# Optimization experiments

Hardware: AMD Instinct MI355X
Metric: run time of the kernel (lower is better)

Reference implementation:

```python
import jax, jax.numpy as jnp
import numpy as np

D_MODEL = 1024
N_HEADS = 16
HEAD_DIM = D_MODEL // N_HEADS


def setup_inputs() -> dict:
    key = jax.random.key(0)
    k_x, k_wqkv, k_bqkv, k_wout, k_bout = jax.random.split(key, 5)
    s = 1.0 / np.sqrt(D_MODEL)
    return {
        "x": jax.random.normal(k_x, (4, 2048, D_MODEL), dtype=jnp.float32),
        "W_qkv": jax.random.normal(k_wqkv, (D_MODEL, 3 * D_MODEL), dtype=jnp.float32) * s,
        "b_qkv": jax.random.normal(k_bqkv, (3 * D_MODEL,), dtype=jnp.float32) * 0.01,
        "W_out": jax.random.normal(k_wout, (D_MODEL, D_MODEL), dtype=jnp.float32) * s,
        "b_out": jax.random.normal(k_bout, (D_MODEL,), dtype=jnp.float32) * 0.01,
    }


def reference(x, W_qkv, b_qkv, W_out, b_out):
    B, T, D = x.shape
    H, Hd = N_HEADS, HEAD_DIM
    qkv = x @ W_qkv + b_qkv                          # [B,T,3D]
    qkv = qkv.reshape(B, T, 3, H, Hd)
    q, k, v = (qkv[:, :, i].transpose(0, 2, 1, 3) for i in range(3))  # [B,H,T,Hd]
    scale = 1.0 / np.sqrt(Hd)
    attn = jnp.einsum("bhqd,bhkd->bhqk", q, k) * scale  # [B,H,T,T]
    causal = jnp.tril(jnp.ones((T, T), dtype=bool))
    attn = jnp.where(causal, attn, -jnp.inf)
    attn = jax.nn.softmax(attn, axis=-1)
    out = jnp.einsum("bhqk,bhkd->bhqd", attn, v)     # [B,H,T,Hd]
    out = out.transpose(0, 2, 1, 3).reshape(B, T, D)
    return out @ W_out + b_out
```

## Files before the change

kernel.cpp:

```cpp
#include <hip/hip_runtime.h>
#include <hip/hip_bf16.h>
#include <string.h>


typedef unsigned short u16;
typedef unsigned int u32;
typedef __bf16 bf16x8 __attribute__((ext_vector_type(8)));
typedef float f32x4 __attribute__((ext_vector_type(4)));

#define MFMA16(a, b, c) __builtin_amdgcn_mfma_f32_16x16x32_bf16((a), (b), (c), 0, 0, 0)

__device__ __forceinline__ u16 f2bf(float f) {
  unsigned u = __float_as_uint(f);
  u += 0x7fffu + ((u >> 16) & 1u);
  return (u16)(u >> 16);
}

__device__ __forceinline__ u32 pk2bf(float a, float b) {
  __hip_bfloat162 h = __float22bfloat162_rn(make_float2(a, b));
  u32 r;
  memcpy(&r, &h, 4);
  return r;
}

__device__ __forceinline__ void gload_lds16(const void* g, void* l) {
  __builtin_amdgcn_global_load_lds((const __attribute__((address_space(1))) void*)g,
                                   (__attribute__((address_space(3))) void*)l, 16, 0, 0);
}

__global__ __launch_bounds__(256) void cast_x_kernel(const float* __restrict__ x,
                                                     u16* __restrict__ xb) {
  int i = blockIdx.x * 256 + threadIdx.x;
  float4 v = ((const float4*)x)[i];
  ushort4 o;
  o.x = f2bf(v.x); o.y = f2bf(v.y); o.z = f2bf(v.z); o.w = f2bf(v.w);
  ((ushort4*)xb)[i] = o;
}

__global__ __launch_bounds__(256) void tcast_kernel(const float* __restrict__ W,
                                                    u16* __restrict__ Wt, int K, int N) {
  __shared__ float tile[32][33];
  int n0 = blockIdx.x * 32, k0 = blockIdx.y * 32;
  int tx = threadIdx.x & 31, ty = threadIdx.x >> 5;
#pragma unroll
  for (int i = 0; i < 4; i++) {
    int k = ty + i * 8;
    tile[k][tx] = W[(size_t)(k0 + k) * N + n0 + tx];
  }
  __syncthreads();
#pragma unroll
  for (int i = 0; i < 4; i++) {
    int n = ty + i * 8;
    Wt[(size_t)(n0 + n) * K + k0 + tx] = f2bf(tile[tx][n]);
  }
}

__global__ __launch_bounds__(512, 2) void gemm_qkv_kernel(const u16* __restrict__ A,
                                                          const u16* __restrict__ Bt,
                                                          const float* __restrict__ bias,
                                                          u16* __restrict__ QKV) {
  __shared__ u16 As[2][256 * 64];
  __shared__ u16 Bs[2][256 * 64];
  const int tid = threadIdx.x, w = tid >> 6, lane = tid & 63;
  const int g = lane >> 4, c = lane & 15;
  const int wr = w >> 2, wc = w & 3;
  const int m0 = blockIdx.y * 256, n0 = blockIdx.x * 256;
  const int srow = lane >> 3;
  const int sch = (lane & 7) ^ srow;
  const int cx = c & 15 & 7;
  const int wrow = w * 8;

  const u16* gA = A + (size_t)(m0 + wrow + srow) * 1024 + sch * 8;
  const u16* gB = Bt + (size_t)(n0 + wrow + srow) * 1024 + sch * 8;

  auto stageA = [&](int buf, int half, int t) {
#pragma unroll
    for (int i = 0; i < 2; i++)
      gload_lds16(gA + (size_t)(half * 128 + i * 64) * 1024 + t * 64,
                  (char*)(As[buf]) + (half * 128 + i * 64 + wrow) * 128);
  };
  auto stageB = [&](int buf, int half, int t) {
#pragma unroll
    for (int i = 0; i < 2; i++)
      gload_lds16(gB + (size_t)(half * 128 + i * 64) * 1024 + t * 64,
                  (char*)(Bs[buf]) + (half * 128 + i * 64 + wrow) * 128);
  };

  f32x4 acc[8][4];
#pragma unroll
  for (int i = 0; i < 8; i++)
#pragma unroll
    for (int j = 0; j < 4; j++) acc[i][j] = (f32x4){0.f, 0.f, 0.f, 0.f};

  stageB(0, 0, 0);
  stageB(0, 1, 0);
  stageA(0, 0, 0);
  stageA(0, 1, 0);
  stageB(1, 0, 1);
  asm volatile("s_waitcnt vmcnt(2)" ::: "memory");
  __builtin_amdgcn_s_barrier();
  __builtin_amdgcn_sched_barrier(0);

  for (int t = 0; t < 16; t++) {
    const int cur = t & 1;
    const u16* Ab = As[cur];
    const u16* Bb = Bs[cur];
    bf16x8 bf[4][2];
#pragma unroll
    for (int q = 0; q < 4; q++) {
      if (q == 0) {
#pragma unroll
        for (int nt = 0; nt < 4; nt++)
#pragma unroll
          for (int kk = 0; kk < 2; kk++)
            bf[nt][kk] = *(const bf16x8*)(Bb + (wc * 64 + nt * 16 + c) * 64 +
                                          ((kk * 4 + g) ^ cx) * 8);
      }
      bf16x8 af[2][2];
#pragma unroll
      for (int mt = 0; mt < 2; mt++)
#pragma unroll
        for (int kk = 0; kk < 2; kk++)
          af[mt][kk] = *(const bf16x8*)(Ab + (wr * 128 + q * 32 + mt * 16 + c) * 64 +
                                        ((kk * 4 + g) ^ cx) * 8);

      if (q == 0) {
        if (t + 1 < 16) stageB((t + 1) & 1, 1, t + 1);
      } else if (q == 1) {
        if (t + 1 < 16) stageA((t + 1) & 1, 0, t + 1);
      } else if (q == 2) {
        if (t + 1 < 16) stageA((t + 1) & 1, 1, t + 1);
      } else {
        if (t + 2 < 16) stageB(t & 1, 0, t + 2);
      }

      __builtin_amdgcn_sched_barrier(0);
      __builtin_amdgcn_s_barrier();
      asm volatile("s_waitcnt lgkmcnt(0)" ::: "memory");
      __builtin_amdgcn_sched_barrier(0);

      __builtin_amdgcn_s_setprio(1);
#pragma unroll
      for (int mt = 0; mt < 2; mt++)
#pragma unroll
        for (int nt = 0; nt < 4; nt++)
#pragma unroll
          for (int kk = 0; kk < 2; kk++)
            acc[q * 2 + mt][nt] = MFMA16(af[mt][kk], bf[nt][kk], acc[q * 2 + mt][nt]);
      __builtin_amdgcn_s_setprio(0);

      if (q == 3) {
        if (t + 2 < 16) {
          asm volatile("s_waitcnt vmcnt(2)" ::: "memory");
        } else if (t + 1 < 16) {
          asm volatile("s_waitcnt vmcnt(0)" ::: "memory");
        }
      }
      __builtin_amdgcn_sched_barrier(0);
      __builtin_amdgcn_s_barrier();
      __builtin_amdgcn_sched_barrier(0);
    }
  }

  const float qscale = (n0 < 1024) ? 0.18033688011112042f : 1.0f;
  float bn[4];
#pragma unroll
  for (int nt = 0; nt < 4; nt++) bn[nt] = bias[n0 + wc * 64 + nt * 16 + c];
#pragma unroll
  for (int mtg = 0; mtg < 8; mtg++) {
#pragma unroll
    for (int r = 0; r < 4; r++) {
      int m = m0 + wr * 128 + mtg * 16 + g * 4 + r;
      int bb = m >> 11, tk = m & 2047;
#pragma unroll
      for (int nt = 0; nt < 4; nt++) {
        int n = n0 + wc * 64 + nt * 16 + c;
        int which = n >> 10, rem = n & 1023, h = rem >> 6, d = rem & 63;
        float v = (acc[mtg][nt][r] + bn[nt]) * qscale;
        QKV[(size_t)which * 8388608 + (((size_t)(bb * 16 + h) * 2048 + tk) * 64 + d)] = f2bf(v);
      }
    }
  }
}

__global__ __launch_bounds__(256) void vtrans_kernel(const u16* __restrict__ V,
                                                     u16* __restrict__ Vt) {
  __shared__ u16 tile[64][65];
  int bh = blockIdx.y;
  int kt = blockIdx.x;
  int t0 = kt * 64;
  int tx = threadIdx.x & 63, ty = threadIdx.x >> 6;
  const u16* src = V + ((size_t)bh * 2048 + t0) * 64;
#pragma unroll
  for (int i = 0; i < 16; i++) {
    int tr = i * 4 + ty;
    tile[tr][tx] = src[tr * 64 + tx];
  }
  __syncthreads();
  u16* dst = Vt + ((size_t)(bh * 32 + kt)) * 4096;
#pragma unroll
  for (int i = 0; i < 16; i++) {
    int d = i * 4 + ty;
    dst[d * 64 + tx] = tile[tx][d];
  }
}

__global__ __launch_bounds__(512, 4) void attn_kernel(const u16* __restrict__ Q,
                                                      const u16* __restrict__ K,
                                                      const u16* __restrict__ Vt,
                                                      u16* __restrict__ ctx) {
  const int pr = blockIdx.x;
  const int qtA = pr, qtB = 15 - pr;
  const int h = blockIdx.y, b = blockIdx.z;
  const int bh = b * 16 + h;
  const int tid = threadIdx.x, w = tid >> 6, lane = tid & 63;
  const int g = lane >> 4, c = lane & 15;

  const u16* Kg = K + (size_t)bh * 2048 * 64;
  const u16* Vg = Vt + (size_t)bh * 32 * 4096;

  __shared__ u16 Ks[2][64 * 64];
  __shared__ u16 Vs[2][64 * 64];
  __shared__ u32 Pw[8][16 * 32];
  u32* pw = Pw[w];

  const int srow = lane >> 3;
  const int schunk = (lane & 7) ^ (srow & 7);
  const int cx = c & 7;
  const int off0 = ((g ^ cx) * 8);
  const int off1 = (((g ^ cx) ^ 4) * 8);
  const int sw = cx << 2;

  bf16x8 onesf;
#pragma unroll
  for (int i = 0; i < 8; i++) onesf[i] = (__bf16)1.0f;

  const u16* QgA = Q + ((size_t)bh * 2048 + qtA * 128) * 64;
  bf16x8 aq0 = *(const bf16x8*)(QgA + (w * 16 + c) * 64 + g * 8);
  bf16x8 aq1 = *(const bf16x8*)(QgA + (w * 16 + c) * 64 + 32 + g * 8);

  {
    int rbase = w * 8;
    gload_lds16(Kg + (size_t)(rbase + srow) * 64 + schunk * 8, (char*)(Ks[0]) + rbase * 128);
    gload_lds16(Vg + (size_t)(rbase + srow) * 64 + schunk * 8, (char*)(Vs[0]) + rbase * 128);
  }
  __syncthreads();

  f32x4 o[4], la;
#pragma unroll
  for (int nt = 0; nt < 4; nt++) o[nt] = (f32x4){0.f, 0.f, 0.f, 0.f};
  la = (f32x4){0.f, 0.f, 0.f, 0.f};

  const int nA = 2 * qtA + 2;

  auto store_tile = [&](int qbase) {
    float inv = 1.f / la[0];
    int q = qbase + w * 16 + c;
    size_t base = ((size_t)(b * 2048 + q)) * 1024 + h * 64;
#pragma unroll
    for (int nt = 0; nt < 4; nt++) {
      u32 lo = pk2bf(o[nt][0] * inv, o[nt][1] * inv);
      u32 hi = pk2bf(o[nt][2] * inv, o[nt][3] * inv);
      *(uint2*)(ctx + base + nt * 16 + g * 4) = make_uint2(lo, hi);
    }
  };

  for (int r = 0; r < 34; r++) {
    if (r) __syncthreads();

    if (r < 33) {
      const int ktn = (r + 1 < nA) ? (r + 1) : (r + 1 - nA);
      const int nb = (r + 1) & 1;
      int rbase = w * 8;
      gload_lds16(Kg + (size_t)ktn * 4096 + (size_t)(rbase + srow) * 64 + schunk * 8,
                  (char*)(Ks[nb]) + rbase * 128);
      gload_lds16(Vg + (size_t)ktn * 4096 + (size_t)(rbase + srow) * 64 + schunk * 8,
                  (char*)(Vs[nb]) + rbase * 128);
    }

    const bool inA = (r < nA);
    const int kt = inA ? r : (r - nA);
    const int qbase = inA ? qtA * 128 : qtB * 128;
    const int sb0 = qbase + w * 16;
    const int kb = kt * 64;

    if (kb <= sb0 + 15) {
      const u16* Kb = Ks[r & 1];
      const u16* Vb = Vs[r & 1];

      f32x4 sa[4];
#pragma unroll
      for (int nt = 0; nt < 4; nt++) {
        bf16x8 k0 = *(const bf16x8*)(Kb + (nt * 16 + c) * 64 + off0);
        bf16x8 k1 = *(const bf16x8*)(Kb + (nt * 16 + c) * 64 + off1);
        f32x4 z = (f32x4){0.f, 0.f, 0.f, 0.f};
        z = MFMA16(k0, aq0, z);
        z = MFMA16(k1, aq1, z);
        sa[nt] = z;
      }

      const bool domask = (kb + 63 > sb0);
      float pe[4][4];
#pragma unroll
      for (int nt = 0; nt < 4; nt++)
#pragma unroll
        for (int rr = 0; rr < 4; rr++) {
          float t = sa[nt][rr];
          if (domask && (kb + nt * 16 + g * 4 + rr) > (sb0 + c)) t = -1e30f;
          pe[nt][rr] = __builtin_amdgcn_exp2f(t);
        }
#pragma unroll
      for (int nt = 0; nt < 4; nt++) {
        u32 lo = pk2bf(pe[nt][0], pe[nt][1]);
        u32 hi = pk2bf(pe[nt][2], pe[nt][3]);
        *(uint2*)(pw + c * 32 + ((nt * 8 + g * 2) ^ sw)) = make_uint2(lo, hi);
      }
      bf16x8 pB0 = *(const bf16x8*)(pw + c * 32 + ((g * 4) ^ sw));
      bf16x8 pB1 = *(const bf16x8*)(pw + c * 32 + ((16 + g * 4) ^ sw));

      la = MFMA16(onesf, pB0, la);
      la = MFMA16(onesf, pB1, la);

#pragma unroll
      for (int nt = 0; nt < 4; nt++) {
        bf16x8 v0 = *(const bf16x8*)(Vb + (nt * 16 + c) * 64 + off0);
        bf16x8 v1 = *(const bf16x8*)(Vb + (nt * 16 + c) * 64 + off1);
        o[nt] = MFMA16(v0, pB0, o[nt]);
        o[nt] = MFMA16(v1, pB1, o[nt]);
      }
    }

    if (r == nA - 1) {
      store_tile(qtA * 128);
#pragma unroll
      for (int nt = 0; nt < 4; nt++) o[nt] = (f32x4){0.f, 0.f, 0.f, 0.f};
      la = (f32x4){0.f, 0.f, 0.f, 0.f};
      const u16* QgB = Q + ((size_t)bh * 2048 + qtB * 128) * 64;
      aq0 = *(const bf16x8*)(QgB + (w * 16 + c) * 64 + g * 8);
      aq1 = *(const bf16x8*)(QgB + (w * 16 + c) * 64 + 32 + g * 8);
    }
  }

  store_tile(qtB * 128);
}

__global__ __launch_bounds__(256) void gemm_proj_kernel(const u16* __restrict__ A,
                                                        const u16* __restrict__ Bt,
                                                        const float* __restrict__ bias,
                                                        float* __restrict__ out) {
  __shared__ u16 As[128 * 64];
  __shared__ u16 Bs[128 * 64];
  const int tid = threadIdx.x, w = tid >> 6, lane = tid & 63;
  const int g = lane >> 4, c = lane & 15;
  const int wr = w >> 1, wc = w & 1;
  const int m0 = blockIdx.y * 128, n0 = blockIdx.x * 128;
  const int srow = lane >> 3;
  const int sch = (lane & 7) ^ srow;
  const int cx = c & 7;

  f32x4 acc[4][4];
#pragma unroll
  for (int i = 0; i < 4; i++)
#pragma unroll
    for (int j = 0; j < 4; j++) acc[i][j] = (f32x4){0.f, 0.f, 0.f, 0.f};

  for (int k0 = 0; k0 < 1024; k0 += 64) {
    __syncthreads();
#pragma unroll
    for (int i = 0; i < 4; i++) {
      int row = w * 32 + i * 8;
      gload_lds16(A + (size_t)(m0 + row + srow) * 1024 + k0 + sch * 8,
                  (char*)As + row * 128);
      gload_lds16(Bt + (size_t)(n0 + row + srow) * 1024 + k0 + sch * 8,
                  (char*)Bs + row * 128);
    }
    __syncthreads();

#pragma unroll
    for (int kk = 0; kk < 2; kk++) {
      bf16x8 af[4], bf[4];
#pragma unroll
      for (int mt = 0; mt < 4; mt++)
        af[mt] = *(const bf16x8*)(As + (wr * 64 + mt * 16 + c) * 64 + ((kk * 4 + g) ^ cx) * 8);
#pragma unroll
      for (int nt = 0; nt < 4; nt++)
        bf[nt] = *(const bf16x8*)(Bs + (wc * 64 + nt * 16 + c) * 64 + ((kk * 4 + g) ^ cx) * 8);
#pragma unroll
      for (int mt = 0; mt < 4; mt++)
#pragma unroll
        for (int nt = 0; nt < 4; nt++) acc[mt][nt] = MFMA16(af[mt], bf[nt], acc[mt][nt]);
    }
  }

  float bn[4];
#pragma unroll
  for (int nt = 0; nt < 4; nt++) bn[nt] = bias[n0 + wc * 64 + nt * 16 + c];
#pragma unroll
  for (int mt = 0; mt < 4; mt++)
#pragma unroll
    for (int r = 0; r < 4; r++) {
      int m = m0 + wr * 64 + mt * 16 + g * 4 + r;
#pragma unroll
      for (int nt = 0; nt < 4; nt++) {
        int n = n0 + wc * 64 + nt * 16 + c;
        out[(size_t)m * 1024 + n] = acc[mt][nt][r] + bn[nt];
      }
    }
}

extern "C" void kernel_launch(void* const* d_in, const int* in_sizes, int n_in,
                              void* d_out, int out_size, void* d_ws, size_t ws_size,
                              hipStream_t stream) {
  const float* x = (const float*)d_in[0];
  const float* Wqkv = (const float*)d_in[1];
  const float* bqkv = (const float*)d_in[2];
  const float* Wout = (const float*)d_in[3];
  const float* bout = (const float*)d_in[4];
  float* out = (float*)d_out;

  char* ws = (char*)d_ws;
  u16* xb  = (u16*)(ws);
  u16* wqt = (u16*)(ws + 16777216);
  u16* wot = (u16*)(ws + 23068672);
  u16* Qb  = (u16*)(ws + 25165824);
  u16* Kb  = Qb + 8388608;
  u16* Vb  = Kb + 8388608;
  u16* Vt  = (u16*)(ws + 75497472);
  u16* ctx = (u16*)(ws + 92274688);

  cast_x_kernel<<<8192, 256, 0, stream>>>(x, xb);
  tcast_kernel<<<dim3(96, 32), 256, 0, stream>>>(Wqkv, wqt, 1024, 3072);
  tcast_kernel<<<dim3(32, 32), 256, 0, stream>>>(Wout, wot, 1024, 1024);
  gemm_qkv_kernel<<<dim3(12, 32), 512, 0, stream>>>(xb, wqt, bqkv, Qb);
  vtrans_kernel<<<dim3(32, 64), 256, 0, stream>>>(Vb, Vt);
  attn_kernel<<<dim3(8, 16, 4), 512, 0, stream>>>(Qb, Kb, Vt, ctx);
  gemm_proj_kernel<<<dim3(8, 64), 256, 0, stream>>>(ctx, wot, bout, out);
}
```

Before: 276.1 us.

## Fuse V transpose into QKV GEMM epilogue and restage loads in quarter tiles

The QKV GEMM epilogue now writes the V third of its output straight into the transposed Vt layout, so the separate vtrans kernel and the round trip of V through global memory are gone. The global-to-LDS staging is also split into quarter-tile loads and rescheduled, with B prefetched two iterations ahead and A partly earlier, and the vmcnt waits are retuned to match. The V writes from the epilogue are strided and less coalesced, and the new waitcnt schedule has to be exactly right to avoid reading LDS before the data has landed.

```diff
diff --git a/kernel.cpp b/kernel.cpp
--- a/kernel.cpp
+++ b/kernel.cpp
@@ -58,7 +58,8 @@
 __global__ __launch_bounds__(512, 2) void gemm_qkv_kernel(const u16* __restrict__ A,
                                                           const u16* __restrict__ Bt,
                                                           const float* __restrict__ bias,
-                                                          u16* __restrict__ QKV) {
+                                                          u16* __restrict__ QKV,
+                                                          u16* __restrict__ Vt) {
   __shared__ u16 As[2][256 * 64];
   __shared__ u16 Bs[2][256 * 64];
   const int tid = threadIdx.x, w = tid >> 6, lane = tid & 63;
@@ -67,23 +68,19 @@
   const int m0 = blockIdx.y * 256, n0 = blockIdx.x * 256;
   const int srow = lane >> 3;
   const int sch = (lane & 7) ^ srow;
-  const int cx = c & 15 & 7;
+  const int cx = c & 7;
   const int wrow = w * 8;
 
   const u16* gA = A + (size_t)(m0 + wrow + srow) * 1024 + sch * 8;
   const u16* gB = Bt + (size_t)(n0 + wrow + srow) * 1024 + sch * 8;
 
-  auto stageA = [&](int buf, int half, int t) {
-#pragma unroll
-    for (int i = 0; i < 2; i++)
-      gload_lds16(gA + (size_t)(half * 128 + i * 64) * 1024 + t * 64,
-                  (char*)(As[buf]) + (half * 128 + i * 64 + wrow) * 128);
+  auto stageAq = [&](int buf, int j, int t) {
+    gload_lds16(gA + (size_t)(j * 64) * 1024 + t * 64,
+                (char*)(As[buf]) + (j * 64 + wrow) * 128);
   };
-  auto stageB = [&](int buf, int half, int t) {
-#pragma unroll
-    for (int i = 0; i < 2; i++)
-      gload_lds16(gB + (size_t)(half * 128 + i * 64) * 1024 + t * 64,
-                  (char*)(Bs[buf]) + (half * 128 + i * 64 + wrow) * 128);
+  auto stageBq = [&](int buf, int j, int t) {
+    gload_lds16(gB + (size_t)(j * 64) * 1024 + t * 64,
+                (char*)(Bs[buf]) + (j * 64 + wrow) * 128);
   };
 
   f32x4 acc[8][4];
@@ -92,12 +89,11 @@
 #pragma unroll
     for (int j = 0; j < 4; j++) acc[i][j] = (f32x4){0.f, 0.f, 0.f, 0.f};
 
-  stageB(0, 0, 0);
-  stageB(0, 1, 0);
-  stageA(0, 0, 0);
-  stageA(0, 1, 0);
-  stageB(1, 0, 1);
-  asm volatile("s_waitcnt vmcnt(2)" ::: "memory");
+  stageBq(0, 0, 0); stageBq(0, 1, 0); stageBq(0, 2, 0); stageBq(0, 3, 0);
+  stageAq(0, 0, 0); stageAq(0, 1, 0); stageAq(0, 2, 0); stageAq(0, 3, 0);
+  stageBq(1, 0, 1); stageBq(1, 1, 1); stageBq(1, 2, 1); stageBq(1, 3, 1);
+  stageAq(1, 0, 1); stageAq(1, 2, 1);
+  asm volatile("s_waitcnt vmcnt(6)" ::: "memory");
   __builtin_amdgcn_s_barrier();
   __builtin_amdgcn_sched_barrier(0);
 
@@ -105,7 +101,7 @@
     const int cur = t & 1;
     const u16* Ab = As[cur];
     const u16* Bb = Bs[cur];
-    bf16x8 bf[4][2];
+    bf16x8 bfr[4][2];
 #pragma unroll
     for (int q = 0; q < 4; q++) {
       if (q == 0) {
@@ -113,8 +109,8 @@
         for (int nt = 0; nt < 4; nt++)
 #pragma unroll
           for (int kk = 0; kk < 2; kk++)
-            bf[nt][kk] = *(const bf16x8*)(Bb + (wc * 64 + nt * 16 + c) * 64 +
-                                          ((kk * 4 + g) ^ cx) * 8);
+            bfr[nt][kk] = *(const bf16x8*)(Bb + (wc * 64 + nt * 16 + c) * 64 +
+                                           ((kk * 4 + g) ^ cx) * 8);
       }
       bf16x8 af[2][2];
 #pragma unroll
@@ -125,13 +121,13 @@
                                         ((kk * 4 + g) ^ cx) * 8);
 
       if (q == 0) {
-        if (t + 1 < 16) stageB((t + 1) & 1, 1, t + 1);
+        if (t + 1 < 16) { stageAq((t + 1) & 1, 1, t + 1); stageAq((t + 1) & 1, 3, t + 1); }
       } else if (q == 1) {
-        if (t + 1 < 16) stageA((t + 1) & 1, 0, t + 1);
+        if (t + 2 < 16) { stageBq(cur, 0, t + 2); stageBq(cur, 1, t + 2); }
       } else if (q == 2) {
-        if (t + 1 < 16) stageA((t + 1) & 1, 1, t + 1);
+        if (t + 2 < 16) { stageBq(cur, 2, t + 2); stageBq(cur, 3, t + 2); }
       } else {
-        if (t + 2 < 16) stageB(t & 1, 0, t + 2);
+        if (t + 2 < 16) { stageAq(cur, 0, t + 2); stageAq(cur, 2, t + 2); }
       }
 
       __builtin_amdgcn_sched_barrier(0);
@@ -146,15 +142,17 @@
         for (int nt = 0; nt < 4; nt++)
 #pragma unroll
           for (int kk = 0; kk < 2; kk++)
-            acc[q * 2 + mt][nt] = MFMA16(af[mt][kk], bf[nt][kk], acc[q * 2 + mt][nt]);
+            acc[q * 2 + mt][nt] = MFMA16(af[mt][kk], bfr[nt][kk], acc[q * 2 + mt][nt]);
       __builtin_amdgcn_s_setprio(0);
 
-      if (q == 3) {
-        if (t + 2 < 16) {
-          asm volatile("s_waitcnt vmcnt(2)" ::: "memory");
-        } else if (t + 1 < 16) {
-          asm volatile("s_waitcnt vmcnt(0)" ::: "memory");
-        }
+      if (q == 1) {
+        if (t < 14)       asm volatile("s_waitcnt vmcnt(10)" ::: "memory");
+        else if (t == 14) asm volatile("s_waitcnt vmcnt(8)" ::: "memory");
+        else              asm volatile("s_waitcnt vmcnt(0)" ::: "memory");
+      } else if (q == 3) {
+        if (t < 14)       asm volatile("s_waitcnt vmcnt(8)" ::: "memory");
+        else if (t == 14) asm volatile("s_waitcnt vmcnt(2)" ::: "memory");
+        else              asm volatile("s_waitcnt vmcnt(0)" ::: "memory");
       }
       __builtin_amdgcn_sched_barrier(0);
       __builtin_amdgcn_s_barrier();
@@ -162,7 +160,8 @@
     }
   }
 
-  const float qscale = (n0 < 1024) ? 0.18033688011112042f : 1.0f;
+  const int which = n0 >> 10;
+  const float qscale = (which == 0) ? 0.18033688011112042f : 1.0f;
   float bn[4];
 #pragma unroll
   for (int nt = 0; nt < 4; nt++) bn[nt] = bias[n0 + wc * 64 + nt * 16 + c];
@@ -175,33 +174,15 @@
 #pragma unroll
       for (int nt = 0; nt < 4; nt++) {
         int n = n0 + wc * 64 + nt * 16 + c;
-        int which = n >> 10, rem = n & 1023, h = rem >> 6, d = rem & 63;
-        float v = (acc[mtg][nt][r] + bn[nt]) * qscale;
-        QKV[(size_t)which * 8388608 + (((size_t)(bb * 16 + h) * 2048 + tk) * 64 + d)] = f2bf(v);
-      }
-    }
-  }
-}
-
-__global__ __launch_bounds__(256) void vtrans_kernel(const u16* __restrict__ V,
-                                                     u16* __restrict__ Vt) {
-  __shared__ u16 tile[64][65];
-  int bh = blockIdx.y;
-  int kt = blockIdx.x;
-  int t0 = kt * 64;
-  int tx = threadIdx.x & 63, ty = threadIdx.x >> 6;
-  const u16* src = V + ((size_t)bh * 2048 + t0) * 64;
-#pragma unroll
-  for (int i = 0; i < 16; i++) {
-    int tr = i * 4 + ty;
-    tile[tr][tx] = src[tr * 64 + tx];
-  }
-  __syncthreads();
-  u16* dst = Vt + ((size_t)(bh * 32 + kt)) * 4096;
-#pragma unroll
-  for (int i = 0; i < 16; i++) {
-    int d = i * 4 + ty;
-    dst[d * 64 + tx] = tile[tx][d];
+        int rem = n & 1023, hh = rem >> 6, d = rem & 63;
+        u16 val = f2bf((acc[mtg][nt][r] + bn[nt]) * qscale);
+        if (which == 2) {
+          Vt[((size_t)(bb * 16 + hh) * 32 + (tk >> 6)) * 4096 + (size_t)d * 64 + (tk & 63)] = val;
+        } else {
+          QKV[(size_t)which * 8388608 + (((size_t)(bb * 16 + hh) * 2048 + tk) * 64 + d)] = val;
+        }
+      }
+    }
   }
 }
 
@@ -424,15 +405,13 @@
   u16* wot = (u16*)(ws + 23068672);
   u16* Qb  = (u16*)(ws + 25165824);
   u16* Kb  = Qb + 8388608;
-  u16* Vb  = Kb + 8388608;
   u16* Vt  = (u16*)(ws + 75497472);
   u16* ctx = (u16*)(ws + 92274688);
 
   cast_x_kernel<<<8192, 256, 0, stream>>>(x, xb);
   tcast_kernel<<<dim3(96, 32), 256, 0, stream>>>(Wqkv, wqt, 1024, 3072);
   tcast_kernel<<<dim3(32, 32), 256, 0, stream>>>(Wout, wot, 1024, 1024);
-  gemm_qkv_kernel<<<dim3(12, 32), 512, 0, stream>>>(xb, wqt, bqkv, Qb);
-  vtrans_kernel<<<dim3(32, 64), 256, 0, stream>>>(Vb, Vt);
+  gemm_qkv_kernel<<<dim3(12, 32), 512, 0, stream>>>(xb, wqt, bqkv, Qb, Vt);
   attn_kernel<<<dim3(8, 16, 4), 512, 0, stream>>>(Qb, Kb, Vt, ctx);
   gemm_proj_kernel<<<dim3(8, 64), 256, 0, stream>>>(ctx, wot, bout, out);
 }
```

Result: slower. 297.6 us (+7.8%).
